# Kernel tuning notes

Hardware: AMD Instinct MI355X
Metric: run time of the kernel (lower is better)

The kernel has to match this reference:

```python
import jax, jax.numpy as jnp
import numpy as np

IN_CH = 512
STYLE_DIM = 512
K_ATT = 4  # block size used in forward()


def make_up_kernel():
    # make_kernel([1,3,3,1]) -> outer product, normalized; Upsample scales by factor**2
    k = jnp.array([1.0, 3.0, 3.0, 1.0], jnp.float32)
    k = k[None, :] * k[:, None]
    k = k / k.sum()
    return k * 4.0  # factor**2 with factor=2


def setup_inputs() -> dict:
    key = jax.random.key(0)
    ks = jax.random.split(key, 8)
    B, H, W = 8, 128, 128
    return {
        "input": jax.random.normal(ks[0], (B, IN_CH, H, W), jnp.float32),
        "style": jax.random.normal(ks[1], (B, STYLE_DIM), jnp.float32),
        "skip": jax.random.normal(ks[2], (B, 3, H // 2, W // 2), jnp.float32),
        "attention0": jax.random.normal(ks[3], (B, 3, H, W), jnp.float32),
        "attention1": jax.random.normal(ks[4], (B, 3, H, W), jnp.float32),
        # learned params
        "conv_w": jax.random.normal(ks[5], (3, IN_CH), jnp.float32),  # ModulatedConv2d weight (1x1 kernel squeezed)
        "mod_w": jax.random.normal(ks[6], (IN_CH, STYLE_DIM), jnp.float32),  # EqualLinear weight
        "mod_b": jnp.ones((IN_CH,), jnp.float32),  # bias_init=1
        "bias": jnp.zeros((1, 3, 1, 1), jnp.float32),
        "q_w": jax.random.normal(ks[7], (1, 3, 3, 3), jnp.float32) * 0.1,  # query_conv weight [O=1,I=3,3,3]
        "q_b": jnp.zeros((1,), jnp.float32),
        "up_kernel": make_up_kernel(),  # registered buffer
    }


def _upsample2x(x, kernel):
    # upfirdn2d(x, kernel, up=2, pad=(2,1)); kernel is symmetric so flip is a no-op.
    # lhs_dilation=2 inserts zeros between samples (length 2H-1); torch's upfirdn also
    # appends one trailing zero, so the right pad becomes pad1+1 = 2.
    C = x.shape[1]
    k = jnp.broadcast_to(kernel[None, None], (C, 1, 4, 4))
    return jax.lax.conv_general_dilated(
        x, k, window_strides=(1, 1), padding=((2, 2), (2, 2)),
        lhs_dilation=(2, 2), feature_group_count=C)


def _conv3x3(x, w, b):
    out = jax.lax.conv_general_dilated(x, w, (1, 1), ((1, 1), (1, 1)))
    return out + b[None, :, None, None]


def _blockify(x, k):
    # F.unfold(x, k, stride=k) for single-channel x: [B,1,H,W] -> [B, k*k, (H/k)*(W/k)]
    B, _, H, W = x.shape
    x = x.reshape(B, H // k, k, W // k, k)
    return x.transpose(0, 2, 4, 1, 3).reshape(B, k * k, (H // k) * (W // k))


def _unblockify(u, k, H, W):
    # F.fold inverse (non-overlapping): [B, k*k, L] -> [B,1,H,W]
    B = u.shape[0]
    x = u.reshape(B, k, k, H // k, W // k)
    return x.transpose(0, 3, 1, 4, 2).reshape(B, 1, H, W)


def _l2norm(u, axes):
    return u / jnp.maximum(jnp.sqrt(jnp.sum(u * u, axis=axes, keepdims=True)), 1e-12)


def reference(input, style, skip, attention0, attention1,
              conv_w, mod_w, mod_b, bias, q_w, q_b, up_kernel):
    B, Cin, H, W = input.shape
    # EqualLinear modulation: scale = 1/sqrt(style_dim)
    s = style @ (mod_w * (1.0 / np.sqrt(STYLE_DIM))).T + mod_b  # [B, Cin]
    # ModulatedConv2d, kernel_size=1, demodulate=False, group=batch conv -> per-sample scaled 1x1 conv
    conv_scale = 1.0 / np.sqrt(Cin)  # fan_in = in_channel * 1**2
    out = jnp.einsum('oi,bi,bihw->bohw', conv_w * conv_scale, s, input) + bias

    # skip path
    skip_up = _upsample2x(skip, up_kernel)

    # attention map (width > k branch, k=4)
    k = K_ATT
    pq = _conv3x3(jax.lax.stop_gradient(attention0), q_w, q_b)  # [B,1,H,W]
    pk = _conv3x3(jax.lax.stop_gradient(attention1), q_w, q_b)
    qu = _l2norm(_blockify(pq, k), axes=1)  # [B, k*k, L], L2 per column (dim=1)
    ku = _l2norm(_blockify(pk, k), axes=1)
    energy = qu * ku
    energy_star = _l2norm(energy, axes=(1, 2)) * k  # F.normalize over dims (1,2), scaled by k
    att = _unblockify(energy_star, k, H, W)  # [B,1,H,W]

    out = out * att + skip_up * (1.0 - att)
    return out
```

## Files before the change

kernel.cpp:

```cpp
#include <hip/hip_runtime.h>
#include <math.h>

#define HW 16384
#define MOD_BLOCKS 1024

__global__ __launch_bounds__(256) void pre_kernel(
    const float* __restrict__ style, const float* __restrict__ mod_w,
    const float* __restrict__ mod_b, const float* __restrict__ conv_w,
    const float* __restrict__ a0in, const float* __restrict__ a1in,
    const float* __restrict__ q_w, const float* __restrict__ q_b,
    float4* __restrict__ weff4, float* __restrict__ energy,
    float* __restrict__ part) {
  int bid = blockIdx.x;
  int t = threadIdx.x;

  if (bid < MOD_BLOCKS) {
    int wg = bid * 4 + (t >> 6);
    int b = wg >> 9;
    int i = wg & 511;
    int lane = t & 63;
    const float4* row = reinterpret_cast<const float4*>(mod_w + (size_t)i * 512);
    const float4* st = reinterpret_cast<const float4*>(style + (size_t)b * 512);
    float4 r0 = row[lane], r1 = row[lane + 64];
    float4 s0 = st[lane], s1 = st[lane + 64];
    float s = r0.x * s0.x + r0.y * s0.y + r0.z * s0.z + r0.w * s0.w +
              r1.x * s1.x + r1.y * s1.y + r1.z * s1.z + r1.w * s1.w;
#pragma unroll
    for (int m = 1; m < 64; m <<= 1) s += __shfl_xor(s, m);
    if (lane == 0) {
      const float kInv = 0.04419417382415922f;
      s = s * kInv + mod_b[i];
      float4 o;
      o.x = conv_w[i] * kInv * s;
      o.y = conv_w[512 + i] * kInv * s;
      o.z = conv_w[1024 + i] * kInv * s;
      o.w = 0.f;
      weff4[(size_t)b * 512 + i] = o;
    }
    return;
  }

  int blk = bid - MOD_BLOCKS;
  int b = blk >> 6;
  int j = blk & 63;
  int colLocal = t >> 4;
  int pos = t & 15;
  int col = j * 16 + colLocal;
  int by = col >> 5, bx = col & 31;
  int iy = pos >> 2, ix = pos & 3;
  int h = by * 4 + iy, w = bx * 4 + ix;

  __shared__ float qw[27];
  __shared__ float qb;
  if (t < 27) qw[t] = q_w[t];
  if (t == 27) qb = q_b[0];
  __syncthreads();

  float pq = qb, pk = qb;
#pragma unroll
  for (int ci = 0; ci < 3; ++ci) {
    const float* p0 = a0in + (size_t)(b * 3 + ci) * HW;
    const float* p1 = a1in + (size_t)(b * 3 + ci) * HW;
#pragma unroll
    for (int ky = 0; ky < 3; ++ky) {
      int hh = h + ky - 1;
      if ((unsigned)hh >= 128u) continue;
#pragma unroll
      for (int kx = 0; kx < 3; ++kx) {
        int ww = w + kx - 1;
        if ((unsigned)ww >= 128u) continue;
        float wq = qw[ci * 9 + ky * 3 + kx];
        pq = fmaf(wq, p0[hh * 128 + ww], pq);
        pk = fmaf(wq, p1[hh * 128 + ww], pk);
      }
    }
  }
  float sq = pq * pq, sk = pk * pk;
#pragma unroll
  for (int m = 1; m < 16; m <<= 1) {
    sq += __shfl_xor(sq, m);
    sk += __shfl_xor(sk, m);
  }
  float qn = 1.0f / fmaxf(sqrtf(sq), 1e-12f);
  float kn = 1.0f / fmaxf(sqrtf(sk), 1e-12f);
  float e = (pq * qn) * (pk * kn);
  energy[(size_t)b * HW + h * 128 + w] = e;

  float ss = e * e;
#pragma unroll
  for (int m = 1; m < 64; m <<= 1) ss += __shfl_xor(ss, m);
  __shared__ float partl[4];
  int wid = t >> 6;
  if ((t & 63) == 0) partl[wid] = ss;
  __syncthreads();
  if (t == 0) part[blk] = partl[0] + partl[1] + partl[2] + partl[3];
}

__global__ __launch_bounds__(256) void main_kernel(
    const float* __restrict__ input, const float4* __restrict__ weff4,
    const float* __restrict__ bias, const float* __restrict__ skip,
    const float* __restrict__ upk, const float* __restrict__ energy,
    const float* __restrict__ part, float* __restrict__ out) {
  __shared__ float4 lw[512];
  __shared__ float ssq_sh;
  int t = threadIdx.x;
  int blk = blockIdx.x;
  int b = blk >> 6;

  const float4* g = weff4 + (size_t)b * 512;
  lw[t] = g[t];
  lw[t + 256] = g[t + 256];
  if (t < 64) {
    float ps = part[b * 64 + t];
#pragma unroll
    for (int m = 1; m < 64; m <<= 1) ps += __shfl_xor(ps, m);
    if (t == 0) ssq_sh = ps;
  }

  int p = (blk & 63) * 256 + t;

  float e = energy[(size_t)b * HW + p];
  int y = p >> 7, x = p & 127;
  int syb = ((y + (y & 1)) >> 1) - 1;
  int sxb = ((x + (x & 1)) >> 1) - 1;
  int ky0 = y & 1, kx0 = x & 1;
  float s0 = 0.f, s1 = 0.f, s2 = 0.f;
#pragma unroll
  for (int a = 0; a < 2; ++a) {
    int sy = syb + a;
    if ((unsigned)sy >= 64u) continue;
#pragma unroll
    for (int c2 = 0; c2 < 2; ++c2) {
      int sx = sxb + c2;
      if ((unsigned)sx >= 64u) continue;
      float kv = upk[(ky0 + 2 * a) * 4 + (kx0 + 2 * c2)];
      size_t base = ((size_t)(b * 3) * 64 + sy) * 64 + sx;
      s0 = fmaf(kv, skip[base], s0);
      s1 = fmaf(kv, skip[base + 4096], s1);
      s2 = fmaf(kv, skip[base + 8192], s2);
    }
  }
  float bi0 = bias[0], bi1 = bias[1], bi2 = bias[2];

  __syncthreads();

  const float* in = input + (size_t)b * 512 * HW + p;
  float a0 = 0.f, a1 = 0.f, a2 = 0.f;
  for (int c0 = 0; c0 < 512; c0 += 32) {
    float v[32];
#pragma unroll
    for (int u = 0; u < 32; ++u) v[u] = in[(size_t)(c0 + u) * HW];
#pragma unroll
    for (int u = 0; u < 32; ++u) {
      float4 w = lw[c0 + u];
      a0 = fmaf(w.x, v[u], a0);
      a1 = fmaf(w.y, v[u], a1);
      a2 = fmaf(w.z, v[u], a2);
    }
  }

  float att = e * (4.0f / fmaxf(sqrtf(ssq_sh), 1e-12f));
  float om = 1.0f - att;
  size_t ob = (size_t)(b * 3) * HW + p;
  out[ob] = (a0 + bi0) * att + s0 * om;
  out[ob + HW] = (a1 + bi1) * att + s1 * om;
  out[ob + 2 * HW] = (a2 + bi2) * att + s2 * om;
}

extern "C" void kernel_launch(void* const* d_in, const int* in_sizes, int n_in,
                              void* d_out, int out_size, void* d_ws,
                              size_t ws_size, hipStream_t stream) {
  const float* input  = (const float*)d_in[0];
  const float* style  = (const float*)d_in[1];
  const float* skip   = (const float*)d_in[2];
  const float* att0   = (const float*)d_in[3];
  const float* att1   = (const float*)d_in[4];
  const float* conv_w = (const float*)d_in[5];
  const float* mod_w  = (const float*)d_in[6];
  const float* mod_b  = (const float*)d_in[7];
  const float* bias   = (const float*)d_in[8];
  const float* q_w    = (const float*)d_in[9];
  const float* q_b    = (const float*)d_in[10];
  const float* upk    = (const float*)d_in[11];

  int B = in_sizes[1] / 512;

  float* ws = (float*)d_ws;
  float4* weff4 = (float4*)ws;
  float* energy = ws + 16384;
  float* part   = ws + 16384 + 131072;

  pre_kernel<<<MOD_BLOCKS + B * 64, 256, 0, stream>>>(
      style, mod_w, mod_b, conv_w, att0, att1, q_w, q_b, weff4, energy, part);
  main_kernel<<<B * 64, 256, 0, stream>>>(input, weff4, bias, skip, upk,
                                          energy, part, (float*)d_out);
}
```

Measured before the change: 56.13 us.

## Fuse pre and main kernels into one cooperative kernel with grid sync

Merges the modulation/energy pre-pass and the main 1x1-conv blend kernel into a single cooperative launch, using a grid-wide sync in place of the kernel boundary. The mod GEMV work is redistributed so each of the 512 blocks computes 8 channels with 32-lane reductions. It also switches the large input reads and output writes to nontemporal loads/stores to avoid cache pollution. This removes one launch and its gap, but adds grid-sync cost and requires all 512 blocks to be co-resident.

```diff
diff --git a/kernel.cpp b/kernel.cpp
--- a/kernel.cpp
+++ b/kernel.cpp
@@ -1,123 +1,122 @@
 #include <hip/hip_runtime.h>
+#include <hip/hip_cooperative_groups.h>
 #include <math.h>
 
 #define HW 16384
-#define MOD_BLOCKS 1024
-
-__global__ __launch_bounds__(256) void pre_kernel(
-    const float* __restrict__ style, const float* __restrict__ mod_w,
-    const float* __restrict__ mod_b, const float* __restrict__ conv_w,
-    const float* __restrict__ a0in, const float* __restrict__ a1in,
-    const float* __restrict__ q_w, const float* __restrict__ q_b,
+
+namespace cg = cooperative_groups;
+
+__global__ __launch_bounds__(256, 2) void fused_kernel(
+    const float* __restrict__ input, const float* __restrict__ style,
+    const float* __restrict__ skip, const float* __restrict__ a0in,
+    const float* __restrict__ a1in, const float* __restrict__ conv_w,
+    const float* __restrict__ mod_w, const float* __restrict__ mod_b,
+    const float* __restrict__ bias, const float* __restrict__ q_w,
+    const float* __restrict__ q_b, const float* __restrict__ upk,
     float4* __restrict__ weff4, float* __restrict__ energy,
-    float* __restrict__ part) {
-  int bid = blockIdx.x;
-  int t = threadIdx.x;
-
-  if (bid < MOD_BLOCKS) {
-    int wg = bid * 4 + (t >> 6);
-    int b = wg >> 9;
-    int i = wg & 511;
-    int lane = t & 63;
-    const float4* row = reinterpret_cast<const float4*>(mod_w + (size_t)i * 512);
-    const float4* st = reinterpret_cast<const float4*>(style + (size_t)b * 512);
-    float4 r0 = row[lane], r1 = row[lane + 64];
-    float4 s0 = st[lane], s1 = st[lane + 64];
-    float s = r0.x * s0.x + r0.y * s0.y + r0.z * s0.z + r0.w * s0.w +
-              r1.x * s1.x + r1.y * s1.y + r1.z * s1.z + r1.w * s1.w;
-#pragma unroll
-    for (int m = 1; m < 64; m <<= 1) s += __shfl_xor(s, m);
-    if (lane == 0) {
-      const float kInv = 0.04419417382415922f;
-      s = s * kInv + mod_b[i];
-      float4 o;
-      o.x = conv_w[i] * kInv * s;
-      o.y = conv_w[512 + i] * kInv * s;
-      o.z = conv_w[1024 + i] * kInv * s;
-      o.w = 0.f;
-      weff4[(size_t)b * 512 + i] = o;
-    }
-    return;
-  }
-
-  int blk = bid - MOD_BLOCKS;
-  int b = blk >> 6;
-  int j = blk & 63;
-  int colLocal = t >> 4;
-  int pos = t & 15;
-  int col = j * 16 + colLocal;
-  int by = col >> 5, bx = col & 31;
-  int iy = pos >> 2, ix = pos & 3;
-  int h = by * 4 + iy, w = bx * 4 + ix;
-
+    float* __restrict__ part, float* __restrict__ out) {
+  __shared__ float4 lw[512];
   __shared__ float qw[27];
   __shared__ float qb;
-  if (t < 27) qw[t] = q_w[t];
-  if (t == 27) qb = q_b[0];
-  __syncthreads();
-
-  float pq = qb, pk = qb;
-#pragma unroll
-  for (int ci = 0; ci < 3; ++ci) {
-    const float* p0 = a0in + (size_t)(b * 3 + ci) * HW;
-    const float* p1 = a1in + (size_t)(b * 3 + ci) * HW;
-#pragma unroll
-    for (int ky = 0; ky < 3; ++ky) {
-      int hh = h + ky - 1;
-      if ((unsigned)hh >= 128u) continue;
-#pragma unroll
-      for (int kx = 0; kx < 3; ++kx) {
-        int ww = w + kx - 1;
-        if ((unsigned)ww >= 128u) continue;
-        float wq = qw[ci * 9 + ky * 3 + kx];
-        pq = fmaf(wq, p0[hh * 128 + ww], pq);
-        pk = fmaf(wq, p1[hh * 128 + ww], pk);
-      }
-    }
-  }
-  float sq = pq * pq, sk = pk * pk;
-#pragma unroll
-  for (int m = 1; m < 16; m <<= 1) {
-    sq += __shfl_xor(sq, m);
-    sk += __shfl_xor(sk, m);
-  }
-  float qn = 1.0f / fmaxf(sqrtf(sq), 1e-12f);
-  float kn = 1.0f / fmaxf(sqrtf(sk), 1e-12f);
-  float e = (pq * qn) * (pk * kn);
-  energy[(size_t)b * HW + h * 128 + w] = e;
-
-  float ss = e * e;
-#pragma unroll
-  for (int m = 1; m < 64; m <<= 1) ss += __shfl_xor(ss, m);
   __shared__ float partl[4];
-  int wid = t >> 6;
-  if ((t & 63) == 0) partl[wid] = ss;
-  __syncthreads();
-  if (t == 0) part[blk] = partl[0] + partl[1] + partl[2] + partl[3];
-}
-
-__global__ __launch_bounds__(256) void main_kernel(
-    const float* __restrict__ input, const float4* __restrict__ weff4,
-    const float* __restrict__ bias, const float* __restrict__ skip,
-    const float* __restrict__ upk, const float* __restrict__ energy,
-    const float* __restrict__ part, float* __restrict__ out) {
-  __shared__ float4 lw[512];
   __shared__ float ssq_sh;
+
   int t = threadIdx.x;
   int blk = blockIdx.x;
   int b = blk >> 6;
-
-  const float4* g = weff4 + (size_t)b * 512;
-  lw[t] = g[t];
-  lw[t + 256] = g[t + 256];
+  int j = blk & 63;
+
+  {
+    int g = t >> 5, l = t & 31;
+    int c = j * 8 + g;
+    const float4* row = reinterpret_cast<const float4*>(mod_w + (size_t)c * 512);
+    const float4* st = reinterpret_cast<const float4*>(style + (size_t)b * 512);
+    float4 r0 = row[l], r1 = row[l + 32], r2 = row[l + 64], r3 = row[l + 96];
+    float4 s0 = st[l], s1 = st[l + 32], s2 = st[l + 64], s3 = st[l + 96];
+    float s = r0.x * s0.x + r0.y * s0.y + r0.z * s0.z + r0.w * s0.w +
+              r1.x * s1.x + r1.y * s1.y + r1.z * s1.z + r1.w * s1.w +
+              r2.x * s2.x + r2.y * s2.y + r2.z * s2.z + r2.w * s2.w +
+              r3.x * s3.x + r3.y * s3.y + r3.z * s3.z + r3.w * s3.w;
+#pragma unroll
+    for (int m = 1; m < 32; m <<= 1) s += __shfl_xor(s, m);
+    if (l == 0) {
+      const float kInv = 0.04419417382415922f;
+      s = s * kInv + mod_b[c];
+      float4 o;
+      o.x = conv_w[c] * kInv * s;
+      o.y = conv_w[512 + c] * kInv * s;
+      o.z = conv_w[1024 + c] * kInv * s;
+      o.w = 0.f;
+      weff4[(size_t)b * 512 + c] = o;
+    }
+  }
+
+  {
+    if (t < 27) qw[t] = q_w[t];
+    if (t == 27) qb = q_b[0];
+    __syncthreads();
+
+    int colLocal = t >> 4;
+    int pos = t & 15;
+    int col = j * 16 + colLocal;
+    int by = col >> 5, bx = col & 31;
+    int iy = pos >> 2, ix = pos & 3;
+    int h = by * 4 + iy, w = bx * 4 + ix;
+
+    float pq = qb, pk = qb;
+#pragma unroll
+    for (int ci = 0; ci < 3; ++ci) {
+      const float* p0 = a0in + (size_t)(b * 3 + ci) * HW;
+      const float* p1 = a1in + (size_t)(b * 3 + ci) * HW;
+#pragma unroll
+      for (int ky = 0; ky < 3; ++ky) {
+        int hh = h + ky - 1;
+        if ((unsigned)hh >= 128u) continue;
+#pragma unroll
+        for (int kx = 0; kx < 3; ++kx) {
+          int ww = w + kx - 1;
+          if ((unsigned)ww >= 128u) continue;
+          float wq = qw[ci * 9 + ky * 3 + kx];
+          pq = fmaf(wq, p0[hh * 128 + ww], pq);
+          pk = fmaf(wq, p1[hh * 128 + ww], pk);
+        }
+      }
+    }
+    float sq = pq * pq, sk = pk * pk;
+#pragma unroll
+    for (int m = 1; m < 16; m <<= 1) {
+      sq += __shfl_xor(sq, m);
+      sk += __shfl_xor(sk, m);
+    }
+    float qn = 1.0f / fmaxf(sqrtf(sq), 1e-12f);
+    float kn = 1.0f / fmaxf(sqrtf(sk), 1e-12f);
+    float e = (pq * qn) * (pk * kn);
+    energy[(size_t)b * HW + h * 128 + w] = e;
+
+    float ss = e * e;
+#pragma unroll
+    for (int m = 1; m < 64; m <<= 1) ss += __shfl_xor(ss, m);
+    int wid = t >> 6;
+    if ((t & 63) == 0) partl[wid] = ss;
+    __syncthreads();
+    if (t == 0) part[blk] = partl[0] + partl[1] + partl[2] + partl[3];
+  }
+
+  __threadfence();
+  cg::this_grid().sync();
+
+  int p = j * 256 + t;
+
+  const float4* g4 = weff4 + (size_t)b * 512;
+  float4 g0 = g4[t], g1 = g4[t + 256];
   if (t < 64) {
     float ps = part[b * 64 + t];
 #pragma unroll
     for (int m = 1; m < 64; m <<= 1) ps += __shfl_xor(ps, m);
     if (t == 0) ssq_sh = ps;
   }
-
-  int p = (blk & 63) * 256 + t;
+  lw[t] = g0;
+  lw[t + 256] = g1;
 
   float e = energy[(size_t)b * HW + p];
   int y = p >> 7, x = p & 127;
@@ -149,7 +148,8 @@
   for (int c0 = 0; c0 < 512; c0 += 32) {
     float v[32];
 #pragma unroll
-    for (int u = 0; u < 32; ++u) v[u] = in[(size_t)(c0 + u) * HW];
+    for (int u = 0; u < 32; ++u)
+      v[u] = __builtin_nontemporal_load(in + (size_t)(c0 + u) * HW);
 #pragma unroll
     for (int u = 0; u < 32; ++u) {
       float4 w = lw[c0 + u];
@@ -162,9 +162,9 @@
   float att = e * (4.0f / fmaxf(sqrtf(ssq_sh), 1e-12f));
   float om = 1.0f - att;
   size_t ob = (size_t)(b * 3) * HW + p;
-  out[ob] = (a0 + bi0) * att + s0 * om;
-  out[ob + HW] = (a1 + bi1) * att + s1 * om;
-  out[ob + 2 * HW] = (a2 + bi2) * att + s2 * om;
+  __builtin_nontemporal_store((a0 + bi0) * att + s0 * om, out + ob);
+  __builtin_nontemporal_store((a1 + bi1) * att + s1 * om, out + ob + HW);
+  __builtin_nontemporal_store((a2 + bi2) * att + s2 * om, out + ob + 2 * HW);
 }
 
 extern "C" void kernel_launch(void* const* d_in, const int* in_sizes, int n_in,
@@ -189,9 +189,13 @@
   float4* weff4 = (float4*)ws;
   float* energy = ws + 16384;
   float* part   = ws + 16384 + 131072;
-
-  pre_kernel<<<MOD_BLOCKS + B * 64, 256, 0, stream>>>(
-      style, mod_w, mod_b, conv_w, att0, att1, q_w, q_b, weff4, energy, part);
-  main_kernel<<<B * 64, 256, 0, stream>>>(input, weff4, bias, skip, upk,
-                                          energy, part, (float*)d_out);
+  float* outp   = (float*)d_out;
+
+  void* args[] = {
+      (void*)&input, (void*)&style, (void*)&skip,  (void*)&att0,
+      (void*)&att1,  (void*)&conv_w, (void*)&mod_w, (void*)&mod_b,
+      (void*)&bias,  (void*)&q_w,    (void*)&q_b,   (void*)&upk,
+      (void*)&weff4, (void*)&energy, (void*)&part,  (void*)&outp};
+  hipLaunchCooperativeKernel((void*)fused_kernel, dim3(B * 64), dim3(256),
+                             args, 0, stream);
 }
```

New measurement: 125.8 us. 2.24x slower.

## Split channel reduction across kernels, overlap modulation with first input channels

Applied to the files above, without the earlier changes.

The first kernel now streams the first 64 input channels per pixel, computing their modulated weights locally (each block recomputes the 64 low weights and a slice of the remaining 448) alongside the attention energy, and writes partial sums to the output. The second kernel loads the precomputed high-channel weights, reads the partial sums back, and finishes the remaining channels and the blend. This aims to hide the small prologue kernel's latency behind useful memory traffic. In exchange it adds redundant mod_w reads in every block and an extra output round trip. Each attention block computation is also duplicated across block pairs.

```diff
diff --git a/kernel.cpp b/kernel.cpp
--- a/kernel.cpp
+++ b/kernel.cpp
@@ -2,65 +2,21 @@
 #include <math.h>
 
 #define HW 16384
-#define MOD_BLOCKS 1024
-
-__global__ __launch_bounds__(256) void pre_kernel(
-    const float* __restrict__ style, const float* __restrict__ mod_w,
-    const float* __restrict__ mod_b, const float* __restrict__ conv_w,
-    const float* __restrict__ a0in, const float* __restrict__ a1in,
-    const float* __restrict__ q_w, const float* __restrict__ q_b,
-    float4* __restrict__ weff4, float* __restrict__ energy,
-    float* __restrict__ part) {
-  int bid = blockIdx.x;
-  int t = threadIdx.x;
-
-  if (bid < MOD_BLOCKS) {
-    int wg = bid * 4 + (t >> 6);
-    int b = wg >> 9;
-    int i = wg & 511;
-    int lane = t & 63;
-    const float4* row = reinterpret_cast<const float4*>(mod_w + (size_t)i * 512);
-    const float4* st = reinterpret_cast<const float4*>(style + (size_t)b * 512);
-    float4 r0 = row[lane], r1 = row[lane + 64];
-    float4 s0 = st[lane], s1 = st[lane + 64];
-    float s = r0.x * s0.x + r0.y * s0.y + r0.z * s0.z + r0.w * s0.w +
-              r1.x * s1.x + r1.y * s1.y + r1.z * s1.z + r1.w * s1.w;
-#pragma unroll
-    for (int m = 1; m < 64; m <<= 1) s += __shfl_xor(s, m);
-    if (lane == 0) {
-      const float kInv = 0.04419417382415922f;
-      s = s * kInv + mod_b[i];
-      float4 o;
-      o.x = conv_w[i] * kInv * s;
-      o.y = conv_w[512 + i] * kInv * s;
-      o.z = conv_w[1024 + i] * kInv * s;
-      o.w = 0.f;
-      weff4[(size_t)b * 512 + i] = o;
-    }
-    return;
-  }
-
-  int blk = bid - MOD_BLOCKS;
-  int b = blk >> 6;
-  int j = blk & 63;
-  int colLocal = t >> 4;
-  int pos = t & 15;
-  int col = j * 16 + colLocal;
-  int by = col >> 5, bx = col & 31;
-  int iy = pos >> 2, ix = pos & 3;
-  int h = by * 4 + iy, w = bx * 4 + ix;
-
-  __shared__ float qw[27];
-  __shared__ float qb;
-  if (t < 27) qw[t] = q_w[t];
-  if (t == 27) qb = q_b[0];
-  __syncthreads();
-
-  float pq = qb, pk = qb;
+#define K1CH 64
+#define SLICE 7
+
+
+__device__ __forceinline__ void conv_pair(const float* __restrict__ p0b,
+                                          const float* __restrict__ p1b,
+                                          const float* __restrict__ qw,
+                                          float qb, int h, int w, float& pq,
+                                          float& pk) {
+  pq = qb;
+  pk = qb;
 #pragma unroll
   for (int ci = 0; ci < 3; ++ci) {
-    const float* p0 = a0in + (size_t)(b * 3 + ci) * HW;
-    const float* p1 = a1in + (size_t)(b * 3 + ci) * HW;
+    const float* p0 = p0b + (size_t)ci * HW;
+    const float* p1 = p1b + (size_t)ci * HW;
 #pragma unroll
     for (int ky = 0; ky < 3; ++ky) {
       int hh = h + ky - 1;
@@ -75,56 +31,176 @@
       }
     }
   }
-  float sq = pq * pq, sk = pk * pk;
-#pragma unroll
-  for (int m = 1; m < 16; m <<= 1) {
-    sq += __shfl_xor(sq, m);
-    sk += __shfl_xor(sk, m);
-  }
-  float qn = 1.0f / fmaxf(sqrtf(sq), 1e-12f);
-  float kn = 1.0f / fmaxf(sqrtf(sk), 1e-12f);
-  float e = (pq * qn) * (pk * kn);
-  energy[(size_t)b * HW + h * 128 + w] = e;
-
-  float ss = e * e;
-#pragma unroll
-  for (int m = 1; m < 64; m <<= 1) ss += __shfl_xor(ss, m);
+}
+
+__global__ __launch_bounds__(256) void k1(
+    const float* __restrict__ input, const float* __restrict__ style,
+    const float* __restrict__ a0in, const float* __restrict__ a1in,
+    const float* __restrict__ conv_w, const float* __restrict__ mod_w,
+    const float* __restrict__ mod_b, const float* __restrict__ q_w,
+    const float* __restrict__ q_b, float* __restrict__ energy,
+    float* __restrict__ part, float4* __restrict__ weffhi,
+    float* __restrict__ outp) {
+  __shared__ __align__(16) float st[512];
+  __shared__ float4 wl[K1CH];
+  __shared__ float qw[27];
+  __shared__ float qb_sh;
   __shared__ float partl[4];
-  int wid = t >> 6;
-  if ((t & 63) == 0) partl[wid] = ss;
+
+  int t = threadIdx.x;
+  int blk = blockIdx.x;
+  int b = blk >> 6, j = blk & 63;
+  int p = j * 256 + t;
+
+  const float* in = input + (size_t)b * 512 * HW + p;
+
+  float va[32], vb[32];
+#pragma unroll
+  for (int u = 0; u < 32; ++u) va[u] = in[(size_t)u * HW];
+#pragma unroll
+  for (int u = 0; u < 32; ++u) vb[u] = in[(size_t)(32 + u) * HW];
+
+  st[t] = style[b * 512 + t];
+  st[t + 256] = style[b * 512 + 256 + t];
+  if (t < 27) qw[t] = q_w[t];
+  if (t == 27) qb_sh = q_b[0];
   __syncthreads();
-  if (t == 0) part[blk] = partl[0] + partl[1] + partl[2] + partl[3];
-}
-
-__global__ __launch_bounds__(256) void main_kernel(
-    const float* __restrict__ input, const float4* __restrict__ weff4,
+
+  const float kInv = 0.04419417382415922f;
+
+  {
+    int c = t >> 2, q = t & 3;
+    const float4* row =
+        reinterpret_cast<const float4*>(mod_w + (size_t)c * 512) + q * 32;
+    const float4* sv = reinterpret_cast<const float4*>(st) + q * 32;
+    float s = 0.f;
+#pragma unroll
+    for (int u = 0; u < 32; ++u) {
+      float4 r = row[u];
+      float4 sx = sv[u];
+      s += r.x * sx.x + r.y * sx.y + r.z * sx.z + r.w * sx.w;
+    }
+    s += __shfl_xor(s, 1);
+    s += __shfl_xor(s, 2);
+    if (q == 0) {
+      float sm = s * kInv + mod_b[c];
+      wl[c] = make_float4(conv_w[c] * kInv * sm, conv_w[512 + c] * kInv * sm,
+                          conv_w[1024 + c] * kInv * sm, 0.f);
+    }
+  }
+
+  if (t < SLICE * 4) {
+    int sI = t >> 2, q = t & 3;
+    int c = K1CH + j * SLICE + sI;
+    const float4* row =
+        reinterpret_cast<const float4*>(mod_w + (size_t)c * 512) + q * 32;
+    const float4* sv = reinterpret_cast<const float4*>(st) + q * 32;
+    float s = 0.f;
+#pragma unroll
+    for (int u = 0; u < 32; ++u) {
+      float4 r = row[u];
+      float4 sx = sv[u];
+      s += r.x * sx.x + r.y * sx.y + r.z * sx.z + r.w * sx.w;
+    }
+    s += __shfl_xor(s, 1);
+    s += __shfl_xor(s, 2);
+    if (q == 0) {
+      float sm = s * kInv + mod_b[c];
+      weffhi[(size_t)b * 448 + (c - K1CH)] =
+          make_float4(conv_w[c] * kInv * sm, conv_w[512 + c] * kInv * sm,
+                      conv_w[1024 + c] * kInv * sm, 0.f);
+    }
+  }
+
+  {
+    int by = j >> 1, bx = t >> 3, sub = t & 7;
+    int hA = 4 * by + (sub >> 2), wA = 4 * bx + (sub & 3);
+    const float* a0b = a0in + (size_t)(b * 3) * HW;
+    const float* a1b = a1in + (size_t)(b * 3) * HW;
+    float pq1, pk1, pq2, pk2;
+    conv_pair(a0b, a1b, qw, qb_sh, hA, wA, pq1, pk1);
+    conv_pair(a0b, a1b, qw, qb_sh, hA + 2, wA, pq2, pk2);
+
+    float s_q = pq1 * pq1 + pq2 * pq2;
+    float s_k = pk1 * pk1 + pk2 * pk2;
+#pragma unroll
+    for (int m = 1; m < 8; m <<= 1) {
+      s_q += __shfl_xor(s_q, m);
+      s_k += __shfl_xor(s_k, m);
+    }
+    float qn = 1.0f / fmaxf(sqrtf(s_q), 1e-12f);
+    float kn = 1.0f / fmaxf(sqrtf(s_k), 1e-12f);
+    float e1 = (pq1 * qn) * (pk1 * kn);
+    float e2 = (pq2 * qn) * (pk2 * kn);
+
+    float own = (j & 1) ? e2 : e1;
+    energy[(size_t)b * HW + (2 * j + (sub >> 2)) * 128 + 4 * bx + (sub & 3)] =
+        own;
+
+    float ss = e1 * e1 + e2 * e2;
+#pragma unroll
+    for (int m = 1; m < 64; m <<= 1) ss += __shfl_xor(ss, m);
+    int wid = t >> 6;
+    if ((t & 63) == 0) partl[wid] = ss;
+  }
+
+  __syncthreads();
+  if (t == 0 && (j & 1) == 0)
+    part[b * 32 + (j >> 1)] = partl[0] + partl[1] + partl[2] + partl[3];
+
+  float A0 = 0.f, A1 = 0.f, A2 = 0.f;
+#pragma unroll
+  for (int u = 0; u < 32; ++u) {
+    float4 w = wl[u];
+    A0 = fmaf(w.x, va[u], A0);
+    A1 = fmaf(w.y, va[u], A1);
+    A2 = fmaf(w.z, va[u], A2);
+  }
+#pragma unroll
+  for (int u = 0; u < 32; ++u) {
+    float4 w = wl[32 + u];
+    A0 = fmaf(w.x, vb[u], A0);
+    A1 = fmaf(w.y, vb[u], A1);
+    A2 = fmaf(w.z, vb[u], A2);
+  }
+  size_t ob = (size_t)(b * 3) * HW + p;
+  outp[ob] = A0;
+  outp[ob + HW] = A1;
+  outp[ob + 2 * HW] = A2;
+}
+
+__global__ __launch_bounds__(256) void k2(
+    const float* __restrict__ input, const float4* __restrict__ weffhi,
     const float* __restrict__ bias, const float* __restrict__ skip,
     const float* __restrict__ upk, const float* __restrict__ energy,
-    const float* __restrict__ part, float* __restrict__ out) {
+    const float* __restrict__ part, float* __restrict__ outp) {
   __shared__ float4 lw[512];
   __shared__ float ssq_sh;
   int t = threadIdx.x;
   int blk = blockIdx.x;
-  int b = blk >> 6;
-
-  const float4* g = weff4 + (size_t)b * 512;
-  lw[t] = g[t];
-  lw[t + 256] = g[t + 256];
-  if (t < 64) {
-    float ps = part[b * 64 + t];
-#pragma unroll
-    for (int m = 1; m < 64; m <<= 1) ps += __shfl_xor(ps, m);
+  int b = blk >> 6, j = blk & 63;
+  int p = j * 256 + t;
+
+  const float4* g = weffhi + (size_t)b * 448;
+  if (t < 224) {
+    lw[64 + t] = g[t];
+    lw[288 + t] = g[224 + t];
+  }
+  if (t < 32) {
+    float ps = part[b * 32 + t];
+#pragma unroll
+    for (int m = 1; m < 32; m <<= 1) ps += __shfl_xor(ps, m);
     if (t == 0) ssq_sh = ps;
   }
 
-  int p = (blk & 63) * 256 + t;
-
   float e = energy[(size_t)b * HW + p];
+  size_t ob = (size_t)(b * 3) * HW + p;
+  float A0 = outp[ob], A1 = outp[ob + HW], A2 = outp[ob + 2 * HW];
   int y = p >> 7, x = p & 127;
   int syb = ((y + (y & 1)) >> 1) - 1;
   int sxb = ((x + (x & 1)) >> 1) - 1;
   int ky0 = y & 1, kx0 = x & 1;
-  float s0 = 0.f, s1 = 0.f, s2 = 0.f;
+  float sk0 = 0.f, sk1 = 0.f, sk2 = 0.f;
 #pragma unroll
   for (int a = 0; a < 2; ++a) {
     int sy = syb + a;
@@ -135,9 +211,9 @@
       if ((unsigned)sx >= 64u) continue;
       float kv = upk[(ky0 + 2 * a) * 4 + (kx0 + 2 * c2)];
       size_t base = ((size_t)(b * 3) * 64 + sy) * 64 + sx;
-      s0 = fmaf(kv, skip[base], s0);
-      s1 = fmaf(kv, skip[base + 4096], s1);
-      s2 = fmaf(kv, skip[base + 8192], s2);
+      sk0 = fmaf(kv, skip[base], sk0);
+      sk1 = fmaf(kv, skip[base + 4096], sk1);
+      sk2 = fmaf(kv, skip[base + 8192], sk2);
     }
   }
   float bi0 = bias[0], bi1 = bias[1], bi2 = bias[2];
@@ -145,26 +221,24 @@
   __syncthreads();
 
   const float* in = input + (size_t)b * 512 * HW + p;
-  float a0 = 0.f, a1 = 0.f, a2 = 0.f;
-  for (int c0 = 0; c0 < 512; c0 += 32) {
+  for (int c0 = 64; c0 < 512; c0 += 32) {
     float v[32];
 #pragma unroll
     for (int u = 0; u < 32; ++u) v[u] = in[(size_t)(c0 + u) * HW];
 #pragma unroll
     for (int u = 0; u < 32; ++u) {
       float4 w = lw[c0 + u];
-      a0 = fmaf(w.x, v[u], a0);
-      a1 = fmaf(w.y, v[u], a1);
-      a2 = fmaf(w.z, v[u], a2);
+      A0 = fmaf(w.x, v[u], A0);
+      A1 = fmaf(w.y, v[u], A1);
+      A2 = fmaf(w.z, v[u], A2);
     }
   }
 
   float att = e * (4.0f / fmaxf(sqrtf(ssq_sh), 1e-12f));
   float om = 1.0f - att;
-  size_t ob = (size_t)(b * 3) * HW + p;
-  out[ob] = (a0 + bi0) * att + s0 * om;
-  out[ob + HW] = (a1 + bi1) * att + s1 * om;
-  out[ob + 2 * HW] = (a2 + bi2) * att + s2 * om;
+  outp[ob] = (A0 + bi0) * att + sk0 * om;
+  outp[ob + HW] = (A1 + bi1) * att + sk1 * om;
+  outp[ob + 2 * HW] = (A2 + bi2) * att + sk2 * om;
 }
 
 extern "C" void kernel_launch(void* const* d_in, const int* in_sizes, int n_in,
@@ -186,12 +260,13 @@
   int B = in_sizes[1] / 512;
 
   float* ws = (float*)d_ws;
-  float4* weff4 = (float4*)ws;
-  float* energy = ws + 16384;
-  float* part   = ws + 16384 + 131072;
-
-  pre_kernel<<<MOD_BLOCKS + B * 64, 256, 0, stream>>>(
-      style, mod_w, mod_b, conv_w, att0, att1, q_w, q_b, weff4, energy, part);
-  main_kernel<<<B * 64, 256, 0, stream>>>(input, weff4, bias, skip, upk,
-                                          energy, part, (float*)d_out);
-}
+  float* energy = ws;
+  float* part   = ws + 131072;
+  float4* weffhi = (float4*)(ws + 131072 + 256);
+  float* outp = (float*)d_out;
+
+  k1<<<B * 64, 256, 0, stream>>>(input, style, att0, att1, conv_w, mod_w,
+                                 mod_b, q_w, q_b, energy, part, weffhi, outp);
+  k2<<<B * 64, 256, 0, stream>>>(input, weffhi, bias, skip, upk, energy, part,
+                                 outp);
+}
```

Result: slower. 70.14 us (+24.9%).
